# Kernel tuning notes

Hardware: AMD Instinct MI355X
Metric: run time of the kernel (lower is better)

## Reference

```python
import jax, jax.numpy as jnp
import numpy as np

B, S = 2048, 40
D, H, DFF = 64, 8, 256


def setup_inputs() -> dict:
    key = jax.random.key(0)
    ks = jax.random.split(key, 32)
    act = jax.random.randint(ks[0], (B, S, 1), 0, 10).astype(jnp.float32)
    zone = jax.random.randint(ks[1], (B, S, 1), 0, 20).astype(jnp.float32)
    rest = jax.random.normal(ks[2], (B, S, 116), dtype=jnp.float32)
    X = jnp.concatenate([act, zone, rest], axis=-1)  # [B,S,118]

    def g(k, shape, scale=0.05):
        return jax.random.normal(k, shape, jnp.float32) * scale

    z = lambda n: jnp.zeros((n,), jnp.float32)
    o = lambda n: jnp.ones((n,), jnp.float32)
    return {
        'X': X,
        'emb_act': g(ks[3], (10, 16), 1.0), 'emb_zone': g(ks[4], (20, 16), 1.0),
        'lin0_W': g(ks[5], (6, 16)), 'lin0_b': z(16),
        'gat_W': g(ks[6], (5, 5)), 'gat_b': z(5), 'gat_a': g(ks[7], (10, 1)),
        'gl0_W': g(ks[8], (110, 64)), 'gl0_b': z(64),
        'gl1_W': g(ks[9], (64, 64)), 'gl1_b': z(64),
        'gl2_W': g(ks[10], (64, 16)), 'gl2_b': z(16),
        'Wqkv': g(ks[11], (D, 3 * D)), 'bqkv': z(3 * D),
        'Wo': g(ks[12], (D, D)), 'bo': z(D),
        'ln1_g': o(D), 'ln1_b': z(D),
        'W1': g(ks[13], (D, DFF)), 'b1': z(DFF),
        'W2': g(ks[14], (DFF, D)), 'b2': z(D),
        'ln2_g': o(D), 'ln2_b': z(D),
        'relu_W': g(ks[15], (D, D)), 'relu_b': z(D),
        'nd_W': g(ks[16], (D, D)), 'nd_b': z(D),
        'ldt_W': g(ks[17], (D, 1)), 'ldt_b': z(1),
        'nz_W': g(ks[18], (D + 1, D + 1)), 'nz_b': z(D + 1),
        'lz_W': g(ks[19], (D + 1, 20)), 'lz_b': z(20),
        'na0_W': g(ks[20], (D + 21, D + 21)), 'na0_b': z(D + 21),
        'na1_W': g(ks[21], (D + 21, D + 21)), 'na1_b': z(D + 21),
        'la_W': g(ks[22], (D + 21, 5)), 'la_b': z(5),
    }


def _ln(x, g, b):
    m = x.mean(-1, keepdims=True)
    v = ((x - m) ** 2).mean(-1, keepdims=True)
    return (x - m) / jnp.sqrt(v + 1e-5) * g + b


def reference(X, emb_act, emb_zone, lin0_W, lin0_b, gat_W, gat_b, gat_a,
              gl0_W, gl0_b, gl1_W, gl1_b, gl2_W, gl2_b,
              Wqkv, bqkv, Wo, bo, ln1_g, ln1_b, W1, b1, W2, b2, ln2_g, ln2_b,
              relu_W, relu_b, nd_W, nd_b, ldt_W, ldt_b,
              nz_W, nz_b, lz_W, lz_b, na0_W, na0_b, na1_W, na1_b, la_W, la_b):
    b, s, _ = X.shape
    act = X[..., 0].astype(jnp.int32)
    zone = X[..., 1].astype(jnp.int32)
    other = X[..., 2:8]
    ff = X[..., 8:]

    Xa = emb_act[act]                       # [B,S,16]
    Xz = emb_zone[zone]                     # [B,S,16]
    od = other @ lin0_W + lin0_b            # [B,S,16]

    # GAT over 22 nodes x 5 feats, vectorized across batch and seq (eval: no dropout)
    h = ff.reshape(b, s, 22, 5) @ gat_W + gat_b          # [B,S,22,5]
    s1 = h @ gat_a[:5, 0]                                # [B,S,22]
    s2 = h @ gat_a[5:, 0]                                # [B,S,22]
    e = jax.nn.leaky_relu(s1[..., :, None] + s2[..., None, :], 0.2)  # [B,S,22,22]
    attn = jax.nn.softmax(e, axis=-1)
    hp = jnp.einsum('bsij,bsjd->bsid', attn, h).reshape(b, s, 110)
    fo = jax.nn.relu(hp @ gl0_W + gl0_b)
    fo = jax.nn.relu(fo @ gl1_W + gl1_b)
    fo = jax.nn.relu(fo @ gl2_W + gl2_b)                 # [B,S,16]

    Xcat = jnp.concatenate([Xa, Xz, od, fo], axis=-1)    # [B,S,64]

    # Faithful replica of the (buggy) positional encoding: zeros_like(src) is 3D,
    # so 'pos' indexes the batch dim and 'i' the seq dim; value is broadcast over features.
    pos = jnp.arange(b, dtype=jnp.float32)[:, None]
    i = jnp.arange(s)
    ang = pos / (100.0 ** (2.0 * i.astype(jnp.float32) / s))
    pe = jnp.where(i % 2 == 0, jnp.sin(ang), jnp.cos(ang))  # [B,S]
    src = Xcat + pe[:, :, None]

    # TransformerEncoderLayer, post-norm, relu, eval mode
    qkv = src @ Wqkv + bqkv
    q, k, v = jnp.split(qkv, 3, axis=-1)
    dh = D // H
    q = q.reshape(b, s, H, dh)
    k = k.reshape(b, s, H, dh)
    v = v.reshape(b, s, H, dh)
    sc = jnp.einsum('bqhd,bkhd->bhqk', q, k) / jnp.sqrt(jnp.float32(dh))
    a = jax.nn.softmax(sc, axis=-1)
    o = jnp.einsum('bhqk,bkhd->bqhd', a, v).reshape(b, s, D) @ Wo + bo
    x = _ln(src + o, ln1_g, ln1_b)
    f = jax.nn.relu(x @ W1 + b1) @ W2 + b2
    x = _ln(x + f, ln2_g, ln2_b)

    xr = x[:, -1] @ relu_W + relu_b                      # [B,64] (no relu, as in source)
    dT = (xr @ nd_W + nd_b) @ ldt_W + ldt_b              # [B,1]
    mz = (jnp.concatenate([dT, xr], 1) @ nz_W + nz_b) @ lz_W + lz_b  # [B,20]
    fa = jnp.concatenate([mz, dT, xr], 1)                # [B,85]
    ma = fa @ na0_W + na0_b
    ma = ma @ na1_W + na1_b
    ma = ma @ la_W + la_b                                # [B,5]
    return jnp.concatenate([dT, mz, ma], 1)              # [B,26]
```

## Files before the change

kernel.cpp:

```cpp
#include <hip/hip_runtime.h>
#include <hip/hip_bf16.h>

typedef __hip_bfloat16 bf16;
typedef float f32x4 __attribute__((ext_vector_type(4)));
typedef short s16x8 __attribute__((ext_vector_type(8)));

#define B_    2048
#define S_    40
#define NTOK  (B_*S_)
#define TPB   256
#define TOKB  64

#define FF_OFF    0
#define A1_OFFD   0
#define A0_OFFD   4288
#define PE_OFFD   8384
#define S2V_OFFD  8448
#define LDS_DW    9920

#define A0B (A0_OFFD*4)
#define A1B (A1_OFFD*4)

#define PK_GL0 0
#define PK_GL1 1024
#define PK_GL2 1536
#define PK_KV  1664
#define PK_TOT 2688

#define H_WQ   0
#define H_WO   512
#define H_W1   1024
#define H_W2   3072
#define H_RELU 5120
#define H_ND   5632
#define H_NZ   6144
#define H_LZ   7104
#define H_NA0  7488
#define H_NA1  8640
#define H_LA   9792
#define H_TOT  9984

__device__ inline unsigned pk2(float a, float b){
    __hip_bfloat16 ha = __float2bfloat16(a), hb = __float2bfloat16(b);
    unsigned short ua = *reinterpret_cast<unsigned short*>(&ha);
    unsigned short ub = *reinterpret_cast<unsigned short*>(&hb);
    return (unsigned)ua | ((unsigned)ub << 16);
}
__device__ inline float blo(unsigned u){ return __uint_as_float(u << 16); }
__device__ inline float bhi(unsigned u){ return __uint_as_float(u & 0xffff0000u); }

__device__ inline float fexp2(float x){
#if __has_builtin(__builtin_amdgcn_exp2f)
    return __builtin_amdgcn_exp2f(x);
#else
    return exp2f(x);
#endif
}

__device__ inline f32x4 MFMA(uint4 a, uint4 b, f32x4 c){
    union { uint4 q; s16x8 s; } A, Bv;
    A.q = a; Bv.q = b;
    return __builtin_amdgcn_mfma_f32_16x16x32_bf16(A.s, Bv.s, c, 0, 0, 0);
}

__device__ inline uint4 packB(const float* W, int ld, int K, int N, int nb, int S, int lane){
    int half = lane >> 4, c15 = lane & 15;
    int col = nb*16 + c15;
    unsigned pr[4];
    #pragma unroll
    for (int jj = 0; jj < 4; ++jj){
        int k0 = S*32 + half*8 + 2*jj;
        float v0 = (k0   < K && col < N) ? W[(size_t)k0*ld + col]     : 0.f;
        float v1 = (k0+1 < K && col < N) ? W[(size_t)(k0+1)*ld + col] : 0.f;
        pr[jj] = pk2(v0, v1);
    }
    return (uint4){pr[0], pr[1], pr[2], pr[3]};
}

__global__ __launch_bounds__(256) void k_pack_all(
    const float* __restrict__ gl0_W, const float* __restrict__ gl1_W,
    const float* __restrict__ gl2_W, const float* __restrict__ Wqkv,
    const float* __restrict__ Wo,    const float* __restrict__ W1,
    const float* __restrict__ W2,    const float* __restrict__ relu_W,
    const float* __restrict__ nd_W,  const float* __restrict__ nz_W,
    const float* __restrict__ lz_W,  const float* __restrict__ na0_W,
    const float* __restrict__ na1_W, const float* __restrict__ la_W,
    uint4* __restrict__ packW, uint4* __restrict__ packH)
{
    int f = blockIdx.x * 256 + threadIdx.x;
    if (f < PK_TOT){
        unsigned pr[4];
        if (f < PK_GL1){
            int w = f >> 8, r = f & 255, S = r >> 6, lane = r & 63;
            int half = lane >> 4, c15 = lane & 15, col = w * 16 + c15;
            #pragma unroll
            for (int jj = 0; jj < 4; ++jj){
                int k0 = S*32 + half*8 + 2*jj;
                float v0 = (k0   < 110) ? gl0_W[k0*64 + col]     : 0.f;
                float v1 = (k0+1 < 110) ? gl0_W[(k0+1)*64 + col] : 0.f;
                pr[jj] = pk2(v0, v1);
            }
        } else if (f < PK_GL2){
            int g = f - PK_GL1, w = g >> 7, r = g & 127, S = r >> 6, lane = r & 63;
            int half = lane >> 4, c15 = lane & 15, col = w * 16 + c15;
            #pragma unroll
            for (int jj = 0; jj < 4; ++jj){
                int k0 = S*32 + half*8 + 2*jj;
                pr[jj] = pk2(gl1_W[k0*64 + col], gl1_W[(k0+1)*64 + col]);
            }
        } else if (f < PK_KV){
            int g = f - PK_GL2, S = g >> 6, lane = g & 63;
            int half = lane >> 4, c15 = lane & 15;
            #pragma unroll
            for (int jj = 0; jj < 4; ++jj){
                int k0 = S*32 + half*8 + 2*jj;
                pr[jj] = pk2(gl2_W[k0*16 + c15], gl2_W[(k0+1)*16 + c15]);
            }
        } else {
            int g = f - PK_KV, w = g >> 8, r = g & 255, cf = r >> 7, r2 = r & 127;
            int S = r2 >> 6, lane = r2 & 63;
            int half = lane >> 4, c15 = lane & 15, col = 64 + w*32 + cf*16 + c15;
            #pragma unroll
            for (int jj = 0; jj < 4; ++jj){
                int k0 = S*32 + half*8 + 2*jj;
                pr[jj] = pk2(Wqkv[k0*192 + col], Wqkv[(k0+1)*192 + col]);
            }
        }
        packW[f] = (uint4){pr[0], pr[1], pr[2], pr[3]};
        return;
    }
    int f2 = f - PK_TOT;
    if (f2 >= H_TOT) return;
    const float* W; int ld, K, N, St, base;
    if      (f2 < H_WO ){ W=Wqkv;   ld=192; K=64;  N=64;  St=2; base=H_WQ;  }
    else if (f2 < H_W1 ){ W=Wo;     ld=64;  K=64;  N=64;  St=2; base=H_WO;  }
    else if (f2 < H_W2 ){ W=W1;     ld=256; K=64;  N=256; St=2; base=H_W1;  }
    else if (f2 < H_RELU){W=W2;     ld=64;  K=256; N=64;  St=8; base=H_W2;  }
    else if (f2 < H_ND ){ W=relu_W; ld=64;  K=64;  N=64;  St=2; base=H_RELU;}
    else if (f2 < H_NZ ){ W=nd_W;   ld=64;  K=64;  N=64;  St=2; base=H_ND;  }
    else if (f2 < H_LZ ){ W=nz_W;   ld=65;  K=65;  N=65;  St=3; base=H_NZ;  }
    else if (f2 < H_NA0){ W=lz_W;   ld=20;  K=65;  N=20;  St=3; base=H_LZ;  }
    else if (f2 < H_NA1){ W=na0_W;  ld=85;  K=85;  N=85;  St=3; base=H_NA0; }
    else if (f2 < H_LA ){ W=na1_W;  ld=85;  K=85;  N=85;  St=3; base=H_NA1; }
    else               { W=la_W;   ld=5;   K=85;  N=5;   St=3; base=H_LA;  }
    int loc = f2 - base;
    int nb = loc / (St*64);
    int rem = loc - nb*St*64;
    packH[f2] = packB(W, ld, K, N, nb, rem >> 6, rem & 63);
}

__global__ __launch_bounds__(TPB) void k_token(
    const float* __restrict__ X,
    const float* __restrict__ emb_act,
    const float* __restrict__ emb_zone,
    const float* __restrict__ lin0_W, const float* __restrict__ lin0_b,
    const float* __restrict__ gat_W,  const float* __restrict__ gat_b,
    const float* __restrict__ gat_a,
    const float* __restrict__ gl0_b,  const float* __restrict__ gl1_b,
    const float* __restrict__ gl2_b,  const float* __restrict__ bqkv,
    const uint4* __restrict__ packW,
    bf16* __restrict__ kv, float* __restrict__ src_last)
{
    __shared__ unsigned L[LDS_DW];
    char* Lb = (char*)L;

    const int t    = threadIdx.x;
    const int w    = t >> 6;
    const int lane = t & 63;
    const int half = (lane >> 4);
    const int c15  = lane & 15;
    const int blk0 = blockIdx.x * TOKB;
    const int swzc = (c15 & 7) << 4;

    for (int task = t; task < TOKB * 22; task += TPB){
        int tt = task / 22;
        int r  = task - tt * 22;
        const float* xp = X + (size_t)(blk0 + tt) * 118 + 8 + r * 5;
        float f0 = xp[0], f1 = xp[1], f2 = xp[2], f3 = xp[3], f4 = xp[4];
        unsigned* dst = &L[FF_OFF + tt * 67 + 3 * r];
        dst[0] = pk2(f0, f1); dst[1] = pk2(f2, f3); dst[2] = pk2(f4, 0.f);
    }
    for (int idx = t; idx < 64 * 9; idx += TPB){
        int row = idx / 9, p = idx - row * 9;
        *(unsigned*)(Lb + A0B + row * 256 + ((220 + 4*p) ^ ((row & 7) << 4))) = 0u;
    }
    float hd[8];
    {
        const float2* xp = (const float2*)(X + (size_t)(blk0 + lane) * 118);
        #pragma unroll
        for (int p = 0; p < 4; ++p){ float2 v = xp[p]; hd[2*p] = v.x; hd[2*p+1] = v.y; }
    }
    if (t < TOKB){
        int tok = blk0 + t;
        int b = tok / 40, s = tok - b * 40;
        float expo = (2.0f * (float)s) / 40.0f;
        float inv100 = fexp2(-expo * 6.6438561897747395f);
        float ang = (float)b * inv100;
        float pe = ((s & 1) == 0) ? __sinf(ang) : __cosf(ang);
        ((float*)&L[PE_OFFD])[t] = pe;
    }
    __syncthreads();

    const float LOG2E = 1.4426950408889634f;
    const unsigned tb = FF_OFF + lane * 67;
    float va1[5], va2[5];
    float cc1 = 0.f, cc2 = 0.f;
    #pragma unroll
    for (int e = 0; e < 5; ++e){
        float u1 = 0.f, u2 = 0.f;
        #pragma unroll
        for (int d = 0; d < 5; ++d){
            u1 += gat_W[e*5+d] * gat_a[d];
            u2 += gat_W[e*5+d] * gat_a[5+d];
        }
        va1[e] = u1 * LOG2E; va2[e] = u2 * LOG2E;
    }
    #pragma unroll
    for (int d = 0; d < 5; ++d){ cc1 += gat_b[d]*gat_a[d]; cc2 += gat_b[d]*gat_a[5+d]; }
    cc1 *= LOG2E; cc2 *= LOG2E;

    {
        float* s2vL = (float*)&L[S2V_OFFD];
        const int njj = (w == 3) ? 4 : 6;
        #pragma unroll
        for (int jj = 0; jj < 6; ++jj){
            if (jj < njj){
                int j = w*6 + jj;
                unsigned u0 = L[tb + 3*j], u1 = L[tb + 3*j + 1], u2 = L[tb + 3*j + 2];
                float f0 = blo(u0), f1 = bhi(u0), f2 = blo(u1), f3 = bhi(u1), f4 = blo(u2);
                s2vL[lane*23 + j] = cc2 + f0*va2[0] + f1*va2[1] + f2*va2[2] + f3*va2[3] + f4*va2[4];
            }
        }
    }
    __syncthreads();

    {
        const float* s2vL = (const float*)&L[S2V_OFFD];
        float s2v[22];
        float m2 = -1e30f;
        #pragma unroll
        for (int j = 0; j < 22; ++j){
            s2v[j] = s2vL[lane*23 + j];
            m2 = fmaxf(m2, s2v[j]);
        }

        const int wbase = w * 6;
        float s1own[6], negmi[6], Z[6], ffp[6][5];
        #pragma unroll
        for (int ii = 0; ii < 6; ++ii){
            int i = wbase + ii; if (i > 21) i = 21;
            unsigned u0 = L[tb + 3*i], u1 = L[tb + 3*i + 1], u2 = L[tb + 3*i + 2];
            float f0 = blo(u0), f1 = bhi(u0), f2 = blo(u1), f3 = bhi(u1), f4 = blo(u2);
            float s1 = cc1 + f0*va1[0] + f1*va1[1] + f2*va1[2] + f3*va1[3] + f4*va1[4];
            s1own[ii] = s1;
            float em = s1 + m2;
            negmi[ii] = -fmaxf(em, 0.2f * em);
            Z[ii] = 0.f;
            #pragma unroll
            for (int e = 0; e < 5; ++e) ffp[ii][e] = 0.f;
        }

        #pragma unroll
        for (int j = 0; j < 22; ++j){
            unsigned u0 = L[tb + 3*j], u1 = L[tb + 3*j + 1], u2 = L[tb + 3*j + 2];
            float f0 = blo(u0), f1 = bhi(u0), f2 = blo(u1), f3 = bhi(u1), f4 = blo(u2);
            float s2j = s2v[j];
            #pragma unroll
            for (int ii = 0; ii < 6; ++ii){
                float e2 = s1own[ii] + s2j;
                float a  = e2 + negmi[ii];
                float bq = fmaf(0.2f, e2, negmi[ii]);
                float wg = fexp2(fmaxf(a, bq));
                Z[ii] += wg;
                ffp[ii][0] = fmaf(wg, f0, ffp[ii][0]);
                ffp[ii][1] = fmaf(wg, f1, ffp[ii][1]);
                ffp[ii][2] = fmaf(wg, f2, ffp[ii][2]);
                ffp[ii][3] = fmaf(wg, f3, ffp[ii][3]);
                ffp[ii][4] = fmaf(wg, f4, ffp[ii][4]);
            }
        }

        const int rswz = (lane & 7) << 4;
        #pragma unroll
        for (int ii = 0; ii < 6; ++ii){
            int i = wbase + ii;
            if (i < 22){
                float rz = 1.f / Z[ii];
                #pragma unroll
                for (int d = 0; d < 5; ++d){
                    float u = 0.f;
                    #pragma unroll
                    for (int e = 0; e < 5; ++e) u += ffp[ii][e] * gat_W[e*5+d];
                    float h = u * rz + gat_b[d];
                    *(bf16*)(Lb + A0B + lane*256 + ((10*i + 2*d) ^ rswz)) = __float2bfloat16(h);
                }
            }
        }
    }
    __syncthreads();

    {
        uint4 bfr[4];
        #pragma unroll
        for (int S = 0; S < 4; ++S) bfr[S] = packW[PK_GL0 + (w*4 + S)*64 + lane];
        const int col = w * 16 + c15;
        float bias = gl0_b[col];
        f32x4 ac0 = {bias,bias,bias,bias}, ac1 = ac0, ac2 = ac0, ac3 = ac0;
        #pragma unroll
        for (int S = 0; S < 4; ++S){
            int koff = S*64 + half*16;
            uint4 a0 = *(const uint4*)(Lb + A0B + (0*16 + c15)*256 + (koff ^ swzc));
            uint4 a1 = *(const uint4*)(Lb + A0B + (1*16 + c15)*256 + (koff ^ swzc));
            uint4 a2 = *(const uint4*)(Lb + A0B + (2*16 + c15)*256 + (koff ^ swzc));
            uint4 a3 = *(const uint4*)(Lb + A0B + (3*16 + c15)*256 + (koff ^ swzc));
            ac0 = MFMA(a0, bfr[S], ac0);
            ac1 = MFMA(a1, bfr[S], ac1);
            ac2 = MFMA(a2, bfr[S], ac2);
            ac3 = MFMA(a3, bfr[S], ac3);
        }
        const int off = col * 2;
        #pragma unroll
        for (int r = 0; r < 4; ++r){
            int row0 = 0*16 + half*4 + r;
            int row1 = 1*16 + half*4 + r;
            int row2 = 2*16 + half*4 + r;
            int row3 = 3*16 + half*4 + r;
            *(bf16*)(Lb + A1B + row0*128 + (off ^ ((row0 & 7) << 4))) = __float2bfloat16(fmaxf(ac0[r], 0.f));
            *(bf16*)(Lb + A1B + row1*128 + (off ^ ((row1 & 7) << 4))) = __float2bfloat16(fmaxf(ac1[r], 0.f));
            *(bf16*)(Lb + A1B + row2*128 + (off ^ ((row2 & 7) << 4))) = __float2bfloat16(fmaxf(ac2[r], 0.f));
            *(bf16*)(Lb + A1B + row3*128 + (off ^ ((row3 & 7) << 4))) = __float2bfloat16(fmaxf(ac3[r], 0.f));
        }
    }
    __syncthreads();

    {
        uint4 bfr[2];
        #pragma unroll
        for (int S = 0; S < 2; ++S) bfr[S] = packW[PK_GL1 + (w*2 + S)*64 + lane];
        const int col = w * 16 + c15;
        float bias = gl1_b[col];
        f32x4 ac0 = {bias,bias,bias,bias}, ac1 = ac0, ac2 = ac0, ac3 = ac0;
        #pragma unroll
        for (int S = 0; S < 2; ++S){
            int koff = S*64 + half*16;
            uint4 a0 = *(const uint4*)(Lb + A1B + (0*16 + c15)*128 + (koff ^ swzc));
            uint4 a1 = *(const uint4*)(Lb + A1B + (1*16 + c15)*128 + (koff ^ swzc));
            uint4 a2 = *(const uint4*)(Lb + A1B + (2*16 + c15)*128 + (koff ^ swzc));
            uint4 a3 = *(const uint4*)(Lb + A1B + (3*16 + c15)*128 + (koff ^ swzc));
            ac0 = MFMA(a0, bfr[S], ac0);
            ac1 = MFMA(a1, bfr[S], ac1);
            ac2 = MFMA(a2, bfr[S], ac2);
            ac3 = MFMA(a3, bfr[S], ac3);
        }
        const int off = col * 2;
        #pragma unroll
        for (int r = 0; r < 4; ++r){
            int row0 = 0*16 + half*4 + r;
            int row1 = 1*16 + half*4 + r;
            int row2 = 2*16 + half*4 + r;
            int row3 = 3*16 + half*4 + r;
            *(bf16*)(Lb + A0B + row0*128 + (off ^ ((row0 & 7) << 4))) = __float2bfloat16(fmaxf(ac0[r], 0.f));
            *(bf16*)(Lb + A0B + row1*128 + (off ^ ((row1 & 7) << 4))) = __float2bfloat16(fmaxf(ac1[r], 0.f));
            *(bf16*)(Lb + A0B + row2*128 + (off ^ ((row2 & 7) << 4))) = __float2bfloat16(fmaxf(ac2[r], 0.f));
            *(bf16*)(Lb + A0B + row3*128 + (off ^ ((row3 & 7) << 4))) = __float2bfloat16(fmaxf(ac3[r], 0.f));
        }
    }
    __syncthreads();

    {
        uint4 bfr[2];
        #pragma unroll
        for (int S = 0; S < 2; ++S) bfr[S] = packW[PK_GL2 + S*64 + lane];
        float bias = gl2_b[c15];
        f32x4 ac = {bias,bias,bias,bias};
        #pragma unroll
        for (int S = 0; S < 2; ++S){
            int koff = S*64 + half*16;
            uint4 a = *(const uint4*)(Lb + A0B + (w*16 + c15)*128 + (koff ^ swzc));
            ac = MFMA(a, bfr[S], ac);
        }
        const float* pef = (const float*)&L[PE_OFFD];
        const int off = (48 + c15) * 2;
        #pragma unroll
        for (int r = 0; r < 4; ++r){
            int row = w*16 + half*4 + r;
            float v = fmaxf(ac[r], 0.f) + pef[row];
            *(bf16*)(Lb + A1B + row*128 + (off ^ ((row & 7) << 4))) = __float2bfloat16(v);
        }

        float pe = pef[lane];
        int ia = (int)hd[0], iz = (int)hd[1];
        const int tswz = (lane & 7) << 4;
        #pragma unroll
        for (int pp = 0; pp < 6; ++pp){
            int p = w * 6 + pp;
            int c0 = 2 * p;
            float v0, v1;
            if (p < 8)        { v0 = emb_act[ia*16 + c0];        v1 = emb_act[ia*16 + c0 + 1]; }
            else if (p < 16)  { v0 = emb_zone[iz*16 + c0 - 16];  v1 = emb_zone[iz*16 + c0 - 15]; }
            else {
                int cc = c0 - 32;
                float o0 = lin0_b[cc], o1 = lin0_b[cc+1];
                #pragma unroll
                for (int e = 0; e < 6; ++e){
                    float f = hd[2 + e];
                    o0 = fmaf(f, lin0_W[e*16 + cc], o0);
                    o1 = fmaf(f, lin0_W[e*16 + cc + 1], o1);
                }
                v0 = o0; v1 = o1;
            }
            *(unsigned*)(Lb + A1B + lane*128 + ((4*p) ^ tswz)) = pk2(v0 + pe, v1 + pe);
        }
    }
    __syncthreads();

    {
        int r0 = 39 - (blk0 % 40);
        if (t < 128){
            int tok = r0 + 40 * (t >> 6);
            if (tok < 64){
                int col = t & 63;
                bf16 hv = *(const bf16*)(Lb + A1B + tok*128 + ((col*2) ^ ((tok & 7) << 4)));
                src_last[(size_t)((blk0 + tok) / 40) * 64 + col] = __bfloat162float(hv);
            }
        }

        uint4 bfk[2][2];
        #pragma unroll
        for (int cf = 0; cf < 2; ++cf)
            #pragma unroll
            for (int S = 0; S < 2; ++S)
                bfk[cf][S] = packW[PK_KV + ((w*2 + cf)*2 + S)*64 + lane];

        float b0v = bqkv[64 + w*32 + c15];
        float b1v = bqkv[64 + w*32 + 16 + c15];
        f32x4 acc[4][2];
        #pragma unroll
        for (int R = 0; R < 4; ++R){
            acc[R][0] = (f32x4){b0v, b0v, b0v, b0v};
            acc[R][1] = (f32x4){b1v, b1v, b1v, b1v};
        }
        #pragma unroll
        for (int S = 0; S < 2; ++S){
            int koff = S*64 + half*16;
            #pragma unroll
            for (int R = 0; R < 4; ++R){
                uint4 a = *(const uint4*)(Lb + A1B + (R*16 + c15)*128 + (koff ^ swzc));
                acc[R][0] = MFMA(a, bfk[0][S], acc[R][0]);
                acc[R][1] = MFMA(a, bfk[1][S], acc[R][1]);
            }
        }
        #pragma unroll
        for (int R = 0; R < 4; ++R){
            #pragma unroll
            for (int cf = 0; cf < 2; ++cf){
                int lcol = w*32 + cf*16 + c15;
                int off = lcol * 2;
                #pragma unroll
                for (int r = 0; r < 4; ++r){
                    int row = R*16 + half*4 + r;
                    *(bf16*)(Lb + A0B + row*256 + (off ^ ((row & 7) << 4))) = __float2bfloat16(acc[R][cf][r]);
                }
            }
        }
    }
    __syncthreads();

    {
        int row = t >> 2;
        int q = t & 3;
        #pragma unroll
        for (int c = 0; c < 4; ++c){
            int chunk = q*4 + c;
            uint4 d = *(const uint4*)(Lb + A0B + row*256 + ((chunk*16) ^ ((row & 7) << 4)));
            *((uint4*)(kv + (size_t)(blk0 + row) * 128 + chunk * 8)) = d;
        }
    }
}

#define T0B 0
#define T1B 8192
#define TQB 16384
#define XRB 24576
#define XFB 32768
#define TFB 40960
#define DTS 57344

#define TBA(base, row, col) (Lb + (base) + (row)*256 + ((((col)*2)) ^ (((row)&7)<<4)))
#define TFA(row, col)       (Lb + TFB   + (row)*512 + ((((col)*2)) ^ (((row)&7)<<4)))
#define XFA(row, col)       (Lb + XFB   + (row)*256 + ((((col)*4)) ^ (((row)&7)<<4)))

#define UNPK(u, arr) { arr[0]=blo(u.x); arr[1]=bhi(u.x); arr[2]=blo(u.y); arr[3]=bhi(u.y); \
                       arr[4]=blo(u.z); arr[5]=bhi(u.z); arr[6]=blo(u.w); arr[7]=bhi(u.w); }

__global__ __launch_bounds__(256) void k_head2(
    const bf16* __restrict__ kv, const float* __restrict__ src_last,
    const uint4* __restrict__ packH,
    const float* __restrict__ bqkv,  const float* __restrict__ bo,
    const float* __restrict__ ln1_g, const float* __restrict__ ln1_b,
    const float* __restrict__ b1,    const float* __restrict__ b2,
    const float* __restrict__ ln2_g, const float* __restrict__ ln2_b,
    const float* __restrict__ relu_b, const float* __restrict__ nd_b,
    const float* __restrict__ ldt_W, const float* __restrict__ ldt_b,
    const float* __restrict__ nz_b,  const float* __restrict__ lz_b,
    const float* __restrict__ na0_b, const float* __restrict__ na1_b,
    const float* __restrict__ la_b,
    float* __restrict__ out)
{
    __shared__ uint4 Lsh[3592];
    char* Lb = (char*)Lsh;
    float* dTs = (float*)(Lb + DTS);

    const int t    = threadIdx.x;
    const int w    = t >> 6;
    const int lane = t & 63;
    const int half = lane >> 4;
    const int c15  = lane & 15;
    const int B0   = blockIdx.x * 32;
    const int bb   = t >> 3;
    const int g    = t & 7;
    const int gb   = B0 + bb;

    {
        const float4* sp = (const float4*)(src_last + (size_t)gb * 64 + g * 8);
        float4 v0 = sp[0], v1 = sp[1];
        *(float4*)XFA(bb, g*8)     = v0;
        *(float4*)XFA(bb, g*8 + 4) = v1;
        uint4 u;
        u.x = pk2(v0.x, v0.y); u.y = pk2(v0.z, v0.w);
        u.z = pk2(v1.x, v1.y); u.w = pk2(v1.z, v1.w);
        *(uint4*)TBA(T0B, bb, g*8) = u;
    }
    __syncthreads();

    {
        int col = w*16 + c15;
        float bias = bqkv[col];
        f32x4 ac0 = {bias,bias,bias,bias}, ac1 = ac0;
        #pragma unroll
        for (int S = 0; S < 2; ++S){
            uint4 bfv = packH[H_WQ + (w*2 + S)*64 + lane];
            uint4 a0 = *(const uint4*)TBA(T0B, c15,      S*32 + half*8);
            uint4 a1 = *(const uint4*)TBA(T0B, 16 + c15, S*32 + half*8);
            ac0 = MFMA(a0, bfv, ac0); ac1 = MFMA(a1, bfv, ac1);
        }
        #pragma unroll
        for (int r = 0; r < 4; ++r){
            *(bf16*)TBA(TQB, half*4 + r,      col) = __float2bfloat16(ac0[r] * 0.35355339059327373f);
            *(bf16*)TBA(TQB, 16 + half*4 + r, col) = __float2bfloat16(ac1[r] * 0.35355339059327373f);
        }
    }
    __syncthreads();

    {
        int pb = t >> 3, h = t & 7;
        int gpb = B0 + pb;
        uint4 qu = *(const uint4*)TBA(TQB, pb, h*8);
        float qh[8]; UNPK(qu, qh);
        const uint4* kp = (const uint4*)(kv + (size_t)gpb * 40 * 128 + h*8);
        const uint4* vp = (const uint4*)(kv + (size_t)gpb * 40 * 128 + 64 + h*8);
        float sc[40];
        float m = -1e30f;
        #pragma unroll 4
        for (int j = 0; j < 40; ++j){
            uint4 ku = kp[j*16];
            float kf[8]; UNPK(ku, kf);
            float a = qh[0]*kf[0] + qh[1]*kf[1] + qh[2]*kf[2] + qh[3]*kf[3]
                    + qh[4]*kf[4] + qh[5]*kf[5] + qh[6]*kf[6] + qh[7]*kf[7];
            sc[j] = a; m = fmaxf(m, a);
        }
        float Z = 0.f;
        float o[8] = {0.f,0.f,0.f,0.f,0.f,0.f,0.f,0.f};
        #pragma unroll 4
        for (int j = 0; j < 40; ++j){
            float wj = __expf(sc[j] - m);
            Z += wj;
            uint4 vu = vp[j*16];
            float vf[8]; UNPK(vu, vf);
            #pragma unroll
            for (int d = 0; d < 8; ++d) o[d] = fmaf(wj, vf[d], o[d]);
        }
        float rz = 1.f / Z;
        uint4 u;
        u.x = pk2(o[0]*rz, o[1]*rz); u.y = pk2(o[2]*rz, o[3]*rz);
        u.z = pk2(o[4]*rz, o[5]*rz); u.w = pk2(o[6]*rz, o[7]*rz);
        *(uint4*)TBA(T1B, pb, h*8) = u;
    }
    __syncthreads();

    {
        int col = w*16 + c15;
        float bias = bo[col];
        f32x4 ac0 = {bias,bias,bias,bias}, ac1 = ac0;
        #pragma unroll
        for (int S = 0; S < 2; ++S){
            uint4 bfv = packH[H_WO + (w*2 + S)*64 + lane];
            uint4 a0 = *(const uint4*)TBA(T1B, c15,      S*32 + half*8);
            uint4 a1 = *(const uint4*)TBA(T1B, 16 + c15, S*32 + half*8);
            ac0 = MFMA(a0, bfv, ac0); ac1 = MFMA(a1, bfv, ac1);
        }
        #pragma unroll
        for (int r = 0; r < 4; ++r){
            *(float*)XFA(half*4 + r,      col) += ac0[r];
            *(float*)XFA(16 + half*4 + r, col) += ac1[r];
        }
    }
    __syncthreads();

    {
        float4 v0 = *(const float4*)XFA(bb, g*8);
        float4 v1 = *(const float4*)XFA(bb, g*8 + 4);
        float vv[8] = {v0.x, v0.y, v0.z, v0.w, v1.x, v1.y, v1.z, v1.w};
        float s = 0.f, s2 = 0.f;
        #pragma unroll
        for (int j = 0; j < 8; ++j){ s += vv[j]; s2 += vv[j]*vv[j]; }
        #pragma unroll
        for (int msk = 1; msk < 8; msk <<= 1){ s += __shfl_xor(s, msk, 8); s2 += __shfl_xor(s2, msk, 8); }
        float mean = s * (1.f/64.f);
        float var  = s2 * (1.f/64.f) - mean*mean;
        float rstd = rsqrtf(var + 1e-5f);
        float xf[8];
        #pragma unroll
        for (int j = 0; j < 8; ++j){
            int c = g*8 + j;
            xf[j] = (vv[j] - mean) * rstd * ln1_g[c] + ln1_b[c];
        }
        uint4 u;
        u.x = pk2(xf[0], xf[1]); u.y = pk2(xf[2], xf[3]);
        u.z = pk2(xf[4], xf[5]); u.w = pk2(xf[6], xf[7]);
        *(uint4*)TBA(T0B, bb, g*8) = u;
        *(float4*)XFA(bb, g*8)     = (float4){xf[0], xf[1], xf[2], xf[3]};
        *(float4*)XFA(bb, g*8 + 4) = (float4){xf[4], xf[5], xf[6], xf[7]};
    }
    __syncthreads();

    {
        uint4 aS[2][2];
        #pragma unroll
        for (int S = 0; S < 2; ++S){
            aS[S][0] = *(const uint4*)TBA(T0B, c15,      S*32 + half*8);
            aS[S][1] = *(const uint4*)TBA(T0B, 16 + c15, S*32 + half*8);
        }
        #pragma unroll
        for (int k = 0; k < 4; ++k){
            int nb = k*4 + w;
            int col = nb*16 + c15;
            float bias = b1[col];
            f32x4 ac0 = {bias,bias,bias,bias}, ac1 = ac0;
            #pragma unroll
            for (int S = 0; S < 2; ++S){
                uint4 bfv = packH[H_W1 + (nb*2 + S)*64 + lane];
                ac0 = MFMA(aS[S][0], bfv, ac0); ac1 = MFMA(aS[S][1], bfv, ac1);
            }
            #pragma unroll
            for (int r = 0; r < 4; ++r){
                *(bf16*)TFA(half*4 + r,      col) = __float2bfloat16(fmaxf(ac0[r], 0.f));
                *(bf16*)TFA(16 + half*4 + r, col) = __float2bfloat16(fmaxf(ac1[r], 0.f));
            }
        }
    }
    __syncthreads();

    {
        int col = w*16 + c15;
        float bias = b2[col];
        f32x4 ac0 = {bias,bias,bias,bias}, ac1 = ac0;
        #pragma unroll
        for (int S = 0; S < 8; ++S){
            uint4 bfv = packH[H_W2 + (w*8 + S)*64 + lane];
            uint4 a0 = *(const uint4*)TFA(c15,      S*32 + half*8);
            uint4 a1 = *(const uint4*)TFA(16 + c15, S*32 + half*8);
            ac0 = MFMA(a0, bfv, ac0); ac1 = MFMA(a1, bfv, ac1);
        }
        #pragma unroll
        for (int r = 0; r < 4; ++r){
            *(float*)XFA(half*4 + r,      col) += ac0[r];
            *(float*)XFA(16 + half*4 + r, col) += ac1[r];
        }
    }
    __syncthreads();

    {
        float4 v0 = *(const float4*)XFA(bb, g*8);
        float4 v1 = *(const float4*)XFA(bb, g*8 + 4);
        float vv[8] = {v0.x, v0.y, v0.z, v0.w, v1.x, v1.y, v1.z, v1.w};
        float s = 0.f, s2 = 0.f;
        #pragma unroll
        for (int j = 0; j < 8; ++j){ s += vv[j]; s2 += vv[j]*vv[j]; }
        #pragma unroll
        for (int msk = 1; msk < 8; msk <<= 1){ s += __shfl_xor(s, msk, 8); s2 += __shfl_xor(s2, msk, 8); }
        float mean = s * (1.f/64.f);
        float var  = s2 * (1.f/64.f) - mean*mean;
        float rstd = rsqrtf(var + 1e-5f);
        float xf[8];
        #pragma unroll
        for (int j = 0; j < 8; ++j){
            int c = g*8 + j;
            xf[j] = (vv[j] - mean) * rstd * ln2_g[c] + ln2_b[c];
        }
        uint4 u;
        u.x = pk2(xf[0], xf[1]); u.y = pk2(xf[2], xf[3]);
        u.z = pk2(xf[4], xf[5]); u.w = pk2(xf[6], xf[7]);
        *(uint4*)TBA(T0B, bb, g*8) = u;
    }
    __syncthreads();

    {
        int col = w*16 + c15;
        float bias = relu_b[col];
        f32x4 ac0 = {bias,bias,bias,bias}, ac1 = ac0;
        #pragma unroll
        for (int S = 0; S < 2; ++S){
            uint4 bfv = packH[H_RELU + (w*2 + S)*64 + lane];
            uint4 a0 = *(const uint4*)TBA(T0B, c15,      S*32 + half*8);
            uint4 a1 = *(const uint4*)TBA(T0B, 16 + c15, S*32 + half*8);
            ac0 = MFMA(a0, bfv, ac0); ac1 = MFMA(a1, bfv, ac1);
        }
        #pragma unroll
        for (int r = 0; r < 4; ++r){
            *(bf16*)TBA(XRB, half*4 + r,      col) = __float2bfloat16(ac0[r]);
            *(bf16*)TBA(XRB, 16 + half*4 + r, col) = __float2bfloat16(ac1[r]);
        }
    }
    __syncthreads();

    {
        int col = w*16 + c15;
        float bias = nd_b[col];
        f32x4 ac0 = {bias,bias,bias,bias}, ac1 = ac0;
        #pragma unroll
        for (int S = 0; S < 2; ++S){
            uint4 bfv = packH[H_ND + (w*2 + S)*64 + lane];
            uint4 a0 = *(const uint4*)TBA(XRB, c15,      S*32 + half*8);
            uint4 a1 = *(const uint4*)TBA(XRB, 16 + c15, S*32 + half*8);
            ac0 = MFMA(a0, bfv, ac0); ac1 = MFMA(a1, bfv, ac1);
        }
        #pragma unroll
        for (int r = 0; r < 4; ++r){
            *(bf16*)TBA(T1B, half*4 + r,      col) = __float2bfloat16(ac0[r]);
            *(bf16*)TBA(T1B, 16 + half*4 + r, col) = __float2bfloat16(ac1[r]);
        }
    }
    __syncthreads();

    {
        uint4 u = *(const uint4*)TBA(T1B, bb, g*8);
        float nf[8]; UNPK(u, nf);
        float p = 0.f;
        #pragma unroll
        for (int j = 0; j < 8; ++j) p = fmaf(nf[j], ldt_W[g*8 + j], p);
        #pragma unroll
        for (int msk = 1; msk < 8; msk <<= 1) p += __shfl_xor(p, msk, 8);
        if (g == 0){
            float dT = p + ldt_b[0];
            dTs[bb] = dT;
            out[(size_t)gb * 26] = dT;
        }
    }
    __syncthreads();

    {
        float dT = dTs[bb];
        for (int c8 = g; c8 < 12; c8 += 8){
            int cb = c8 * 8;
            unsigned pr[4];
            #pragma unroll
            for (int pj = 0; pj < 4; ++pj){
                int c0 = cb + 2*pj, c1 = c0 + 1;
                float v0 = (c0 == 0) ? dT :
                           (c0 <= 64 ? __bfloat162float(*(const bf16*)TBA(XRB, bb, c0-1)) : 0.f);
                float v1 = (c1 <= 64 ? __bfloat162float(*(const bf16*)TBA(XRB, bb, c1-1)) : 0.f);
                pr[pj] = pk2(v0, v1);
            }
            *(uint4*)TBA(T0B, bb, cb) = (uint4){pr[0], pr[1], pr[2], pr[3]};
        }
    }
    __syncthreads();

    {
        uint4 aS[3][2];
        #pragma unroll
        for (int S = 0; S < 3; ++S){
            aS[S][0] = *(const uint4*)TBA(T0B, c15,      S*32 + half*8);
            aS[S][1] = *(const uint4*)TBA(T0B, 16 + c15, S*32 + half*8);
        }
        int nbl[2]; int nnb = 1; nbl[0] = w;
        if (w == 0){ nbl[1] = 4; nnb = 2; }
        for (int q = 0; q < nnb; ++q){
            int nb = nbl[q];
            int col = nb*16 + c15;
            float bias = (col < 65) ? nz_b[col] : 0.f;
            f32x4 ac0 = {bias,bias,bias,bias}, ac1 = ac0;
            #pragma unroll
            for (int S = 0; S < 3; ++S){
                uint4 bfv = packH[H_NZ + (nb*3 + S)*64 + lane];
                ac0 = MFMA(aS[S][0], bfv, ac0); ac1 = MFMA(aS[S][1], bfv, ac1);
            }
            #pragma unroll
            for (int r = 0; r < 4; ++r){
                *(bf16*)TBA(T1B, half*4 + r,      col) = __float2bfloat16(ac0[r]);
                *(bf16*)TBA(T1B, 16 + half*4 + r, col) = __float2bfloat16(ac1[r]);
            }
        }
        if (t < 64){
            int row = t >> 1, seg = t & 1;
            *(uint4*)TBA(T1B, row, 80 + seg*8) = (uint4){0u,0u,0u,0u};
        }
    }
    __syncthreads();

    if (w < 2){
        uint4 aS[3][2];
        #pragma unroll
        for (int S = 0; S < 3; ++S){
            aS[S][0] = *(const uint4*)TBA(T1B, c15,      S*32 + half*8);
            aS[S][1] = *(const uint4*)TBA(T1B, 16 + c15, S*32 + half*8);
        }
        int nb = w;
        int col = nb*16 + c15;
        float bias = (col < 20) ? lz_b[col] : 0.f;
        f32x4 ac0 = {bias,bias,bias,bias}, ac1 = ac0;
        #pragma unroll
        for (int S = 0; S < 3; ++S){
            uint4 bfv = packH[H_LZ + (nb*3 + S)*64 + lane];
            ac0 = MFMA(aS[S][0], bfv, ac0); ac1 = MFMA(aS[S][1], bfv, ac1);
        }
        #pragma unroll
        for (int r = 0; r < 4; ++r){
            int r0 = half*4 + r, r1 = 16 + half*4 + r;
            *(bf16*)TBA(TQB, r0, col) = __float2bfloat16(ac0[r]);
            *(bf16*)TBA(TQB, r1, col) = __float2bfloat16(ac1[r]);
            if (col < 20){
                out[(size_t)(B0 + r0) * 26 + 1 + col] = ac0[r];
                out[(size_t)(B0 + r1) * 26 + 1 + col] = ac1[r];
            }
        }
    }
    __syncthreads();

    {
        float dT = dTs[bb];
        for (int c8 = g; c8 < 12; c8 += 8){
            int cb = c8 * 8;
            unsigned pr[4];
            #pragma unroll
            for (int pj = 0; pj < 4; ++pj){
                float vv[2];
                #pragma unroll
                for (int hh = 0; hh < 2; ++hh){
                    int c = cb + 2*pj + hh;
                    float v;
                    if (c < 20)       v = __bfloat162float(*(const bf16*)TBA(TQB, bb, c));
                    else if (c == 20) v = dT;
                    else if (c < 85)  v = __bfloat162float(*(const bf16*)TBA(XRB, bb, c - 21));
                    else              v = 0.f;
                    vv[hh] = v;
                }
                pr[pj] = pk2(vv[0], vv[1]);
            }
            *(uint4*)TBA(T0B, bb, cb) = (uint4){pr[0], pr[1], pr[2], pr[3]};
        }
    }
    __syncthreads();

    {
        uint4 aS[3][2];
        #pragma unroll
        for (int S = 0; S < 3; ++S){
            aS[S][0] = *(const uint4*)TBA(T0B, c15,      S*32 + half*8);
            aS[S][1] = *(const uint4*)TBA(T0B, 16 + c15, S*32 + half*8);
        }
        int nbl[2]; int nnb = 1; nbl[0] = w;
        if (w < 2){ nbl[1] = 4 + w; nnb = 2; }
        for (int q = 0; q < nnb; ++q){
            int nb = nbl[q];
            int col = nb*16 + c15;
            float bias = (col < 85) ? na0_b[col] : 0.f;
            f32x4 ac0 = {bias,bias,bias,bias}, ac1 = ac0;
            #pragma unroll
            for (int S = 0; S < 3; ++S){
                uint4 bfv = packH[H_NA0 + (nb*3 + S)*64 + lane];
                ac0 = MFMA(aS[S][0], bfv, ac0); ac1 = MFMA(aS[S][1], bfv, ac1);
            }
            #pragma unroll
            for (int r = 0; r < 4; ++r){
                *(bf16*)TBA(T1B, half*4 + r,      col) = __float2bfloat16(ac0[r]);
                *(bf16*)TBA(T1B, 16 + half*4 + r, col) = __float2bfloat16(ac1[r]);
            }
        }
    }
    __syncthreads();

    {
        uint4 aS[3][2];
        #pragma unroll
        for (int S = 0; S < 3; ++S){
            aS[S][0] = *(const uint4*)TBA(T1B, c15,      S*32 + half*8);
            aS[S][1] = *(const uint4*)TBA(T1B, 16 + c15, S*32 + half*8);
        }
        int nbl[2]; int nnb = 1; nbl[0] = w;
        if (w < 2){ nbl[1] = 4 + w; nnb = 2; }
        for (int q = 0; q < nnb; ++q){
            int nb = nbl[q];
            int col = nb*16 + c15;
            float bias = (col < 85) ? na1_b[col] : 0.f;
            f32x4 ac0 = {bias,bias,bias,bias}, ac1 = ac0;
            #pragma unroll
            for (int S = 0; S < 3; ++S){
                uint4 bfv = packH[H_NA1 + (nb*3 + S)*64 + lane];
                ac0 = MFMA(aS[S][0], bfv, ac0); ac1 = MFMA(aS[S][1], bfv, ac1);
            }
            #pragma unroll
            for (int r = 0; r < 4; ++r){
                *(bf16*)TBA(T0B, half*4 + r,      col) = __float2bfloat16(ac0[r]);
                *(bf16*)TBA(T0B, 16 + half*4 + r, col) = __float2bfloat16(ac1[r]);
            }
        }
    }
    __syncthreads();

    if (w == 0){
        int col = c15;
        float bias = (col < 5) ? la_b[col] : 0.f;
        f32x4 ac0 = {bias,bias,bias,bias}, ac1 = ac0;
        #pragma unroll
        for (int S = 0; S < 3; ++S){
            uint4 bfv = packH[H_LA + S*64 + lane];
            uint4 a0 = *(const uint4*)TBA(T0B, c15,      S*32 + half*8);
            uint4 a1 = *(const uint4*)TBA(T0B, 16 + c15, S*32 + half*8);
            ac0 = MFMA(a0, bfv, ac0); ac1 = MFMA(a1, bfv, ac1);
        }
        if (col < 5){
            #pragma unroll
            for (int r = 0; r < 4; ++r){
                out[(size_t)(B0 + half*4 + r) * 26 + 21 + col]      = ac0[r];
                out[(size_t)(B0 + 16 + half*4 + r) * 26 + 21 + col] = ac1[r];
            }
        }
    }
}

extern "C" void kernel_launch(void* const* d_in, const int* in_sizes, int n_in,
                              void* d_out, int out_size, void* d_ws, size_t ws_size,
                              hipStream_t stream)
{
    const float* X        = (const float*)d_in[0];
    const float* emb_act  = (const float*)d_in[1];
    const float* emb_zone = (const float*)d_in[2];
    const float* lin0_W   = (const float*)d_in[3];
    const float* lin0_b   = (const float*)d_in[4];
    const float* gat_W    = (const float*)d_in[5];
    const float* gat_b    = (const float*)d_in[6];
    const float* gat_a    = (const float*)d_in[7];
    const float* gl0_W    = (const float*)d_in[8];
    const float* gl0_b    = (const float*)d_in[9];
    const float* gl1_W    = (const float*)d_in[10];
    const float* gl1_b    = (const float*)d_in[11];
    const float* gl2_W    = (const float*)d_in[12];
    const float* gl2_b    = (const float*)d_in[13];
    const float* Wqkv     = (const float*)d_in[14];
    const float* bqkv     = (const float*)d_in[15];
    const float* Wo       = (const float*)d_in[16];
    const float* bo       = (const float*)d_in[17];
    const float* ln1_g    = (const float*)d_in[18];
    const float* ln1_b    = (const float*)d_in[19];
    const float* W1       = (const float*)d_in[20];
    const float* b1       = (const float*)d_in[21];
    const float* W2       = (const float*)d_in[22];
    const float* b2       = (const float*)d_in[23];
    const float* ln2_g    = (const float*)d_in[24];
    const float* ln2_b    = (const float*)d_in[25];
    const float* relu_W   = (const float*)d_in[26];
    const float* relu_b   = (const float*)d_in[27];
    const float* nd_W     = (const float*)d_in[28];
    const float* nd_b     = (const float*)d_in[29];
    const float* ldt_W    = (const float*)d_in[30];
    const float* ldt_b    = (const float*)d_in[31];
    const float* nz_W     = (const float*)d_in[32];
    const float* nz_b     = (const float*)d_in[33];
    const float* lz_W     = (const float*)d_in[34];
    const float* lz_b     = (const float*)d_in[35];
    const float* na0_W    = (const float*)d_in[36];
    const float* na0_b    = (const float*)d_in[37];
    const float* na1_W    = (const float*)d_in[38];
    const float* na1_b    = (const float*)d_in[39];
    const float* la_W     = (const float*)d_in[40];
    const float* la_b     = (const float*)d_in[41];

    char* wsb = (char*)d_ws;
    bf16*  kv       = (bf16*)wsb;
    float* src_last = (float*)(wsb + (size_t)NTOK * 128 * sizeof(bf16));
    uint4* packW    = (uint4*)(wsb + (size_t)NTOK * 128 * sizeof(bf16) + (size_t)B_ * 64 * sizeof(float));
    uint4* packH    = packW + PK_TOT;

    k_pack_all<<<(PK_TOT + H_TOT + 255)/256, 256, 0, stream>>>(
        gl0_W, gl1_W, gl2_W, Wqkv, Wo, W1, W2, relu_W, nd_W, nz_W, lz_W,
        na0_W, na1_W, la_W, packW, packH);

    k_token<<<NTOK/TOKB, TPB, 0, stream>>>(X, emb_act, emb_zone, lin0_W, lin0_b,
        gat_W, gat_b, gat_a, gl0_b, gl1_b, gl2_b, bqkv, packW, kv, src_last);

    k_head2<<<B_/32, 256, 0, stream>>>(kv, src_last, packH, bqkv, bo,
        ln1_g, ln1_b, b1, b2, ln2_g, ln2_b, relu_b, nd_b, ldt_W, ldt_b,
        nz_b, lz_b, na0_b, na1_b, la_b, (float*)d_out);
}
```

Before: 76.78 us.

## Pack GAT features densely, recompute s2 inline, stage token header in LDS

The 110 GAT input features per token are now loaded as float2 pairs and packed densely into 55 dwords per token instead of 67 padded dwords. The separate s2 precompute pass, its LDS buffer and one barrier are removed, and s2 is recomputed per neighbour from the packed features. The per-token header (indices and six continuous features) is staged in LDS by the first 64 threads rather than loaded into registers by every thread. This reduces LDS footprint, global load instructions and synchronisation, at the cost of extra ALU work for recomputing s2 and odd/even unpacking logic.

```diff
diff --git a/kernel.cpp b/kernel.cpp
--- a/kernel.cpp
+++ b/kernel.cpp
@@ -13,10 +13,11 @@
 
 #define FF_OFF    0
 #define A1_OFFD   0
-#define A0_OFFD   4288
-#define PE_OFFD   8384
-#define S2V_OFFD  8448
-#define LDS_DW    9920
+#define A0_OFFD   3520
+#define PE_OFFD   7616
+#define IA_OFFD   7680
+#define HD_OFFD   7744
+#define LDS_DW    8128
 
 #define A0B (A0_OFFD*4)
 #define A1B (A1_OFFD*4)
@@ -61,6 +62,16 @@
     union { uint4 q; s16x8 s; } A, Bv;
     A.q = a; Bv.q = b;
     return __builtin_amdgcn_mfma_f32_16x16x32_bf16(A.s, Bv.s, c, 0, 0, 0);
+}
+
+__device__ inline void ldff(const unsigned* L, unsigned tb, int j, float f[5]){
+    int k = (5*j) >> 1;
+    unsigned u0 = L[tb + k], u1 = L[tb + k + 1], u2 = L[tb + k + 2];
+    if ((j & 1) == 0){
+        f[0]=blo(u0); f[1]=bhi(u0); f[2]=blo(u1); f[3]=bhi(u1); f[4]=blo(u2);
+    } else {
+        f[0]=bhi(u0); f[1]=blo(u1); f[2]=bhi(u1); f[3]=blo(u2); f[4]=bhi(u2);
+    }
 }
 
 __device__ inline uint4 packB(const float* W, int ld, int K, int N, int nb, int S, int lane){
@@ -172,76 +183,64 @@
     const int blk0 = blockIdx.x * TOKB;
     const int swzc = (c15 & 7) << 4;
 
-    for (int task = t; task < TOKB * 22; task += TPB){
-        int tt = task / 22;
-        int r  = task - tt * 22;
-        const float* xp = X + (size_t)(blk0 + tt) * 118 + 8 + r * 5;
-        float f0 = xp[0], f1 = xp[1], f2 = xp[2], f3 = xp[3], f4 = xp[4];
-        unsigned* dst = &L[FF_OFF + tt * 67 + 3 * r];
-        dst[0] = pk2(f0, f1); dst[1] = pk2(f2, f3); dst[2] = pk2(f4, 0.f);
+    for (int task = t; task < TOKB * 11; task += TPB){
+        int tt = task / 11;
+        int p  = task - tt * 11;
+        const float2* xp = (const float2*)(X + (size_t)(blk0 + tt) * 118 + 8 + 10 * p);
+        float2 a0 = xp[0], a1 = xp[1], a2 = xp[2], a3 = xp[3], a4 = xp[4];
+        unsigned* dst = &L[FF_OFF + tt * 55 + 5 * p];
+        dst[0] = pk2(a0.x, a0.y);
+        dst[1] = pk2(a1.x, a1.y);
+        dst[2] = pk2(a2.x, a2.y);
+        dst[3] = pk2(a3.x, a3.y);
+        dst[4] = pk2(a4.x, a4.y);
     }
     for (int idx = t; idx < 64 * 9; idx += TPB){
         int row = idx / 9, p = idx - row * 9;
         *(unsigned*)(Lb + A0B + row * 256 + ((220 + 4*p) ^ ((row & 7) << 4))) = 0u;
     }
-    float hd[8];
-    {
-        const float2* xp = (const float2*)(X + (size_t)(blk0 + lane) * 118);
-        #pragma unroll
-        for (int p = 0; p < 4; ++p){ float2 v = xp[p]; hd[2*p] = v.x; hd[2*p+1] = v.y; }
-    }
     if (t < TOKB){
         int tok = blk0 + t;
+        const float2* xp = (const float2*)(X + (size_t)tok * 118);
+        float2 v0 = xp[0], v1 = xp[1], v2 = xp[2], v3 = xp[3];
         int b = tok / 40, s = tok - b * 40;
         float expo = (2.0f * (float)s) / 40.0f;
         float inv100 = fexp2(-expo * 6.6438561897747395f);
         float ang = (float)b * inv100;
         float pe = ((s & 1) == 0) ? __sinf(ang) : __cosf(ang);
         ((float*)&L[PE_OFFD])[t] = pe;
-    }
-    __syncthreads();
-
-    const float LOG2E = 1.4426950408889634f;
-    const unsigned tb = FF_OFF + lane * 67;
-    float va1[5], va2[5];
-    float cc1 = 0.f, cc2 = 0.f;
-    #pragma unroll
-    for (int e = 0; e < 5; ++e){
-        float u1 = 0.f, u2 = 0.f;
-        #pragma unroll
-        for (int d = 0; d < 5; ++d){
-            u1 += gat_W[e*5+d] * gat_a[d];
-            u2 += gat_W[e*5+d] * gat_a[5+d];
-        }
-        va1[e] = u1 * LOG2E; va2[e] = u2 * LOG2E;
-    }
-    #pragma unroll
-    for (int d = 0; d < 5; ++d){ cc1 += gat_b[d]*gat_a[d]; cc2 += gat_b[d]*gat_a[5+d]; }
-    cc1 *= LOG2E; cc2 *= LOG2E;
-
-    {
-        float* s2vL = (float*)&L[S2V_OFFD];
-        const int njj = (w == 3) ? 4 : 6;
-        #pragma unroll
-        for (int jj = 0; jj < 6; ++jj){
-            if (jj < njj){
-                int j = w*6 + jj;
-                unsigned u0 = L[tb + 3*j], u1 = L[tb + 3*j + 1], u2 = L[tb + 3*j + 2];
-                float f0 = blo(u0), f1 = bhi(u0), f2 = blo(u1), f3 = bhi(u1), f4 = blo(u2);
-                s2vL[lane*23 + j] = cc2 + f0*va2[0] + f1*va2[1] + f2*va2[2] + f3*va2[3] + f4*va2[4];
-            }
-        }
-    }
-    __syncthreads();
-
-    {
-        const float* s2vL = (const float*)&L[S2V_OFFD];
-        float s2v[22];
+        L[IA_OFFD + t] = (((unsigned)(int)v0.x) << 16) | ((unsigned)(int)v0.y & 0xffffu);
+        float* hdL = (float*)&L[HD_OFFD + t * 6];
+        hdL[0] = v1.x; hdL[1] = v1.y; hdL[2] = v2.x;
+        hdL[3] = v2.y; hdL[4] = v3.x; hdL[5] = v3.y;
+    }
+    __syncthreads();
+
+    {
+        const float LOG2E = 1.4426950408889634f;
+        const unsigned tb = FF_OFF + lane * 55;
+        float va1[5], va2[5];
+        float cc1 = 0.f, cc2 = 0.f;
+        #pragma unroll
+        for (int e = 0; e < 5; ++e){
+            float u1 = 0.f, u2 = 0.f;
+            #pragma unroll
+            for (int d = 0; d < 5; ++d){
+                u1 += gat_W[e*5+d] * gat_a[d];
+                u2 += gat_W[e*5+d] * gat_a[5+d];
+            }
+            va1[e] = u1 * LOG2E; va2[e] = u2 * LOG2E;
+        }
+        #pragma unroll
+        for (int d = 0; d < 5; ++d){ cc1 += gat_b[d]*gat_a[d]; cc2 += gat_b[d]*gat_a[5+d]; }
+        cc1 *= LOG2E; cc2 *= LOG2E;
+
         float m2 = -1e30f;
         #pragma unroll
         for (int j = 0; j < 22; ++j){
-            s2v[j] = s2vL[lane*23 + j];
-            m2 = fmaxf(m2, s2v[j]);
+            float f[5]; ldff(L, tb, j, f);
+            float s2j = cc2 + f[0]*va2[0] + f[1]*va2[1] + f[2]*va2[2] + f[3]*va2[3] + f[4]*va2[4];
+            m2 = fmaxf(m2, s2j);
         }
 
         const int wbase = w * 6;
@@ -249,9 +248,8 @@
         #pragma unroll
         for (int ii = 0; ii < 6; ++ii){
             int i = wbase + ii; if (i > 21) i = 21;
-            unsigned u0 = L[tb + 3*i], u1 = L[tb + 3*i + 1], u2 = L[tb + 3*i + 2];
-            float f0 = blo(u0), f1 = bhi(u0), f2 = blo(u1), f3 = bhi(u1), f4 = blo(u2);
-            float s1 = cc1 + f0*va1[0] + f1*va1[1] + f2*va1[2] + f3*va1[3] + f4*va1[4];
+            float f[5]; ldff(L, tb, i, f);
+            float s1 = cc1 + f[0]*va1[0] + f[1]*va1[1] + f[2]*va1[2] + f[3]*va1[3] + f[4]*va1[4];
             s1own[ii] = s1;
             float em = s1 + m2;
             negmi[ii] = -fmaxf(em, 0.2f * em);
@@ -262,9 +260,8 @@
 
         #pragma unroll
         for (int j = 0; j < 22; ++j){
-            unsigned u0 = L[tb + 3*j], u1 = L[tb + 3*j + 1], u2 = L[tb + 3*j + 2];
-            float f0 = blo(u0), f1 = bhi(u0), f2 = blo(u1), f3 = bhi(u1), f4 = blo(u2);
-            float s2j = s2v[j];
+            float f[5]; ldff(L, tb, j, f);
+            float s2j = cc2 + f[0]*va2[0] + f[1]*va2[1] + f[2]*va2[2] + f[3]*va2[3] + f[4]*va2[4];
             #pragma unroll
             for (int ii = 0; ii < 6; ++ii){
                 float e2 = s1own[ii] + s2j;
@@ -272,11 +269,11 @@
                 float bq = fmaf(0.2f, e2, negmi[ii]);
                 float wg = fexp2(fmaxf(a, bq));
                 Z[ii] += wg;
-                ffp[ii][0] = fmaf(wg, f0, ffp[ii][0]);
-                ffp[ii][1] = fmaf(wg, f1, ffp[ii][1]);
-                ffp[ii][2] = fmaf(wg, f2, ffp[ii][2]);
-                ffp[ii][3] = fmaf(wg, f3, ffp[ii][3]);
-                ffp[ii][4] = fmaf(wg, f4, ffp[ii][4]);
+                ffp[ii][0] = fmaf(wg, f[0], ffp[ii][0]);
+                ffp[ii][1] = fmaf(wg, f[1], ffp[ii][1]);
+                ffp[ii][2] = fmaf(wg, f[2], ffp[ii][2]);
+                ffp[ii][3] = fmaf(wg, f[3], ffp[ii][3]);
+                ffp[ii][4] = fmaf(wg, f[4], ffp[ii][4]);
             }
         }
 
@@ -389,7 +386,9 @@
         }
 
         float pe = pef[lane];
-        int ia = (int)hd[0], iz = (int)hd[1];
+        unsigned iaz = L[IA_OFFD + lane];
+        int ia = (int)(iaz >> 16), iz = (int)(iaz & 0xffffu);
+        const float* hdL = (const float*)&L[HD_OFFD + lane * 6];
         const int tswz = (lane & 7) << 4;
         #pragma unroll
         for (int pp = 0; pp < 6; ++pp){
@@ -403,7 +402,7 @@
                 float o0 = lin0_b[cc], o1 = lin0_b[cc+1];
                 #pragma unroll
                 for (int e = 0; e < 6; ++e){
-                    float f = hd[2 + e];
+                    float f = hdL[e];
                     o0 = fmaf(f, lin0_W[e*16 + cc], o0);
                     o1 = fmaf(f, lin0_W[e*16 + cc + 1], o1);
                 }
```

Measured after the change: 74.43 us. 3.1% less time.
